# Kernel optimization log

Hardware: AMD Instinct MI355X
Metric: run time of the kernel (lower is better)

## Reference

```python
import jax, jax.numpy as jnp
import numpy as np

EPS = 1e-12  # F.normalize default eps


def build_graph(src, tgt):
    # src,tgt: (b, wh, c). torch does this under no_grad -> stop_gradient.
    logits = jnp.einsum('bnc,bmc->bnm', src, tgt)      # (b, wh, wh)
    g = jax.nn.softmax(logits, axis=-1)                # row softmax
    g = g / jnp.clip(jnp.sum(jnp.abs(g), axis=-2, keepdims=True), EPS)  # L1 norm over dim=-2
    return jax.lax.stop_gradient(g)


def gconv(A, source, message, Wa, ba, Wu, bu):
    # Gconv (PCA-GM style): A @ relu(Linear_a(message)) + relu(Linear_u(source))
    ax = jax.nn.relu(jnp.einsum('bnc,cd->bnd', message, Wa) + ba)
    ux = jax.nn.relu(jnp.einsum('bnc,cd->bnd', source, Wu) + bu)
    return jnp.einsum('bnm,bmd->bnd', A, ax) + ux


def setup_inputs() -> dict:
    key = jax.random.key(0)
    ks = jax.random.split(key, 10)
    b, c, h, w = 4, 256, 64, 64
    scale = 1.0 / np.sqrt(c)
    inp = {
        'skt': jax.random.normal(ks[0], (b, c, h, w), jnp.float32),
        'ref': jax.random.normal(ks[1], (b, c, h, w), jnp.float32),
        'Wa3': jax.random.normal(ks[2], (c, c), jnp.float32) * scale,
        'ba3': jnp.zeros((c,), jnp.float32),
        'Wu3': jax.random.normal(ks[3], (c, c), jnp.float32) * scale,
        'bu3': jnp.zeros((c,), jnp.float32),
        'Wa4': jax.random.normal(ks[4], (c, c), jnp.float32) * scale,
        'ba4': jnp.zeros((c,), jnp.float32),
        'Wu4': jax.random.normal(ks[5], (c, c), jnp.float32) * scale,
        'bu4': jnp.zeros((c,), jnp.float32),
    }
    return inp


def reference(skt, ref, Wa3, ba3, Wu3, bu3, Wa4, ba4, Wu4, bu4):
    b, c, h, w = skt.shape
    skt_f = skt.reshape(b, c, h * w).transpose(0, 2, 1)  # (b, wh, c)
    ref_f = ref.reshape(b, c, h * w).transpose(0, 2, 1)
    sr = build_graph(skt_f, ref_f)                       # (b, wh, wh)
    gen = gconv(sr, skt_f, ref_f, Wa3, ba3, Wu3, bu3) + skt_f
    gg = build_graph(gen, gen)
    ggen = gconv(gg, gen, gen, Wa4, ba4, Wu4, bu4) + gen
    return ggen
```

## Files before the change

### kernel.cpp

```cpp
#include <hip/hip_runtime.h>
#include <cstdint>
#include <cstddef>

#define WH 4096
#define CD 256
typedef long long i64;

typedef __attribute__((ext_vector_type(8))) _Float16 f16x8;
typedef __attribute__((ext_vector_type(4))) float f32x4;

#define AS1 __attribute__((address_space(1)))
#define AS3 __attribute__((address_space(3)))

__device__ __forceinline__ unsigned short f2h(float f) {
    _Float16 h = (_Float16)f;
    return __builtin_bit_cast(unsigned short, h);
}
__device__ __forceinline__ float h2f(unsigned short u) {
    return (float)__builtin_bit_cast(_Float16, u);
}
__device__ __forceinline__ void ld16_lds(const void* g, void* l) {
    __builtin_amdgcn_global_load_lds((AS1 void*)g, (AS3 void*)l, 16, 0, 0);
}

__global__ __launch_bounds__(256) void k_trans(const float* __restrict__ src,
                                               unsigned short* __restrict__ dhi,
                                               unsigned short* __restrict__ dlo,
                                               int RR, int CC, i64 ss, i64 ds) {
    __shared__ float t[32][33];
    const float* s = src + (i64)blockIdx.z * ss;
    const int c0 = blockIdx.x * 32, r0 = blockIdx.y * 32;
    const int tx = threadIdx.x, ty = threadIdx.y;
#pragma unroll
    for (int i = 0; i < 4; ++i)
        t[ty + i * 8][tx] = s[(i64)(r0 + ty + i * 8) * CC + c0 + tx];
    __syncthreads();
#pragma unroll
    for (int i = 0; i < 4; ++i) {
        const i64 idx = (i64)blockIdx.z * ds + (i64)(c0 + ty + i * 8) * RR + r0 + tx;
        const float v = t[tx][ty + i * 8];
        const unsigned short hi = f2h(v);
        dhi[idx] = hi;
        dlo[idx] = f2h(v - h2f(hi));
    }
}

template <int MODE, int SPLIT3>
__global__ __launch_bounds__(256) void k_gemm(
    const unsigned short* __restrict__ A, const unsigned short* __restrict__ A2, int lda, i64 sA,
    const unsigned short* __restrict__ B, const unsigned short* __restrict__ B2, int ldb, i64 sB,
    float* __restrict__ Cf, unsigned short* __restrict__ Chi, unsigned short* __restrict__ Clo,
    int ldc, i64 sC, int K,
    const float* __restrict__ bias,
    const unsigned short* __restrict__ addh, const unsigned short* __restrict__ addl,
    float2* __restrict__ rowP) {
    __shared__ __align__(16) short lA[SPLIT3 ? 8192 : 4096];
    __shared__ __align__(16) short lB[SPLIT3 ? 8192 : 4096];
    __shared__ float2 redp[2][128];
    const int z = blockIdx.z;
    A += (i64)z * sA; B += (i64)z * sB;
    if constexpr (SPLIT3) { A2 += (i64)z * sA; B2 += (i64)z * sB; }

    const int tid = threadIdx.x;
    const int w = tid >> 6, l = tid & 63;
    const int wm = w >> 1, wn = w & 1;
    const int bm = blockIdx.y * 128, bn = blockIdx.x * 128;
    const int l15 = l & 15, lq = l >> 4;

    f32x4 acc[4][4] = {};

    for (int kt = 0; kt < K; kt += 32) {
        __syncthreads();
#pragma unroll
        for (int rr = 0; rr < 2; ++rr) {
            const int r = w + rr * 4;
            const int kb = r >> 1, mh = r & 1;
            const int row = mh * 64 + l;
            const i64 ao = (i64)(bm + row) * lda + kt + kb * 8;
            const i64 bo = (i64)(bn + row) * ldb + kt + kb * 8;
            ld16_lds(A + ao, (char*)lA + r * 1024);
            ld16_lds(B + bo, (char*)lB + r * 1024);
            if constexpr (SPLIT3) {
                ld16_lds(A2 + ao, (char*)lA + 8192 + r * 1024);
                ld16_lds(B2 + bo, (char*)lB + 8192 + r * 1024);
            }
        }
        __syncthreads();
        f16x8 ah[4], bh[4], al[4], bl[4];
#pragma unroll
        for (int i = 0; i < 4; ++i) {
            const int ia = (lq * 128 + wm * 64 + i * 16 + l15) * 8;
            const int ib = (lq * 128 + wn * 64 + i * 16 + l15) * 8;
            ah[i] = *(const f16x8*)(lA + ia);
            bh[i] = *(const f16x8*)(lB + ib);
            if constexpr (SPLIT3) {
                al[i] = *(const f16x8*)(lA + 4096 + ia);
                bl[i] = *(const f16x8*)(lB + 4096 + ib);
            }
        }
#pragma unroll
        for (int i = 0; i < 4; ++i)
#pragma unroll
            for (int j = 0; j < 4; ++j) {
                acc[i][j] = __builtin_amdgcn_mfma_f32_16x16x32_f16(ah[i], bh[j], acc[i][j], 0, 0, 0);
                if constexpr (SPLIT3) {
                    acc[i][j] = __builtin_amdgcn_mfma_f32_16x16x32_f16(ah[i], bl[j], acc[i][j], 0, 0, 0);
                    acc[i][j] = __builtin_amdgcn_mfma_f32_16x16x32_f16(al[i], bh[j], acc[i][j], 0, 0, 0);
                }
            }
    }

#pragma unroll
    for (int i = 0; i < 4; ++i)
#pragma unroll
        for (int j = 0; j < 4; ++j) {
            const int n = bn + wn * 64 + j * 16 + l15;
            const int m0 = bm + wm * 64 + i * 16 + lq * 4;
            float bv = 0.f;
            if constexpr (MODE == 1 || MODE == 2) bv = bias[n];
            if constexpr (MODE == 1) {
                unsigned short hv[4], lv[4];
#pragma unroll
                for (int r = 0; r < 4; ++r) {
                    const float v = fmaxf(acc[i][j][r] + bv, 0.f);
                    hv[r] = f2h(v);
                    lv[r] = f2h(v - h2f(hv[r]));
                }
                const i64 tb = (i64)z * sC + (i64)n * ldc + m0;
                *(ushort4*)(Chi + tb) = make_ushort4(hv[0], hv[1], hv[2], hv[3]);
                *(ushort4*)(Clo + tb) = make_ushort4(lv[0], lv[1], lv[2], lv[3]);
            } else {
#pragma unroll
                for (int r = 0; r < 4; ++r) {
                    float v = acc[i][j][r];
                    const i64 idx = (i64)z * sC + (i64)(m0 + r) * ldc + n;
                    if constexpr (MODE == 0) {
                        Cf[idx] = v;
                    } else {
                        v = fmaxf(v + bv, 0.f);
                        v += h2f(addh[idx]) + h2f(addl[idx]);
                        Cf[idx] = v;
                    }
                }
            }
        }

    if constexpr (MODE == 0) {
        float rm[16], rs[16];
#pragma unroll
        for (int i = 0; i < 4; ++i)
#pragma unroll
            for (int r = 0; r < 4; ++r) {
                float m = fmaxf(fmaxf(acc[i][0][r], acc[i][1][r]), fmaxf(acc[i][2][r], acc[i][3][r]));
                m = fmaxf(m, __shfl_xor(m, 1));
                m = fmaxf(m, __shfl_xor(m, 2));
                m = fmaxf(m, __shfl_xor(m, 4));
                m = fmaxf(m, __shfl_xor(m, 8));
                rm[i * 4 + r] = m;
                float s = __expf(acc[i][0][r] - m) + __expf(acc[i][1][r] - m)
                        + __expf(acc[i][2][r] - m) + __expf(acc[i][3][r] - m);
                s += __shfl_xor(s, 1); s += __shfl_xor(s, 2);
                s += __shfl_xor(s, 4); s += __shfl_xor(s, 8);
                rs[i * 4 + r] = s;
            }
        __syncthreads();
        if (l15 == 0) {
#pragma unroll
            for (int i = 0; i < 4; ++i)
#pragma unroll
                for (int r = 0; r < 4; ++r)
                    redp[wn][wm * 64 + i * 16 + lq * 4 + r] = make_float2(rm[i * 4 + r], rs[i * 4 + r]);
        }
        __syncthreads();
        if (tid < 128) {
            const float2 a = redp[0][tid], b = redp[1][tid];
            const float m = fmaxf(a.x, b.x);
            const float s = a.y * __expf(a.x - m) + b.y * __expf(b.x - m);
            rowP[(i64)blockIdx.x * WH + bm + tid] = make_float2(m, s);
        }
    }
}

__global__ __launch_bounds__(256) void k_colpart(const float* __restrict__ L,
                                                 const float2* __restrict__ rowP,
                                                 float* __restrict__ o,
                                                 float* __restrict__ part) {
    __shared__ float os[64];
    const int t = threadIdx.x;
    const int r0 = blockIdx.y * 64;
    if (t < 64) {
        float M = -3.4e38f, S = 0.f;
        for (int x = 0; x < 32; ++x) {
            const float2 p = rowP[(i64)x * WH + r0 + t];
            const float nm = fmaxf(M, p.x);
            S = S * __expf(M - nm) + p.y * __expf(p.x - nm);
            M = nm;
        }
        const float ov = M + __logf(S);
        os[t] = ov;
        if (blockIdx.x == 0) o[r0 + t] = ov;
    }
    __syncthreads();
    const int j = blockIdx.x * 256 + t;
    float ps = 0.f;
    for (int r = 0; r < 64; ++r)
        ps += __expf(L[(i64)(r0 + r) * WH + j] - os[r]);
    part[(i64)blockIdx.y * WH + j] = ps;
}

__global__ __launch_bounds__(256) void k_colreduce(const float* __restrict__ part,
                                                   float* __restrict__ colS) {
    const int j = blockIdx.x * 256 + threadIdx.x;
    float C = 0.f;
    for (int rb = 0; rb < 64; ++rb) C += part[(i64)rb * WH + j];
    colS[j] = 1.f / fmaxf(C, 1e-12f);
}

template <int FULL>
__global__ __launch_bounds__(256) void k_attn(
    const float* __restrict__ L, const float* __restrict__ o,
    const float* __restrict__ colS,
    const unsigned short* __restrict__ Bh, const unsigned short* __restrict__ Bl,
    unsigned short* __restrict__ Pw) {
    __shared__ __align__(16) float lL[4096];
    __shared__ __align__(16) short lBh[4096];
    __shared__ __align__(16) short lBl[FULL ? 4096 : 64];
    __shared__ float lS[512];
    const int tid = threadIdx.x;
    const int w = tid >> 6, l = tid & 63;
    const int wm = w >> 1, wn = w & 1;
    const int bm = blockIdx.y * 128, bn = blockIdx.x * 128;
    const int l15 = l & 15, lq = l >> 4;
    const i64 koff = (i64)blockIdx.z * 512;

#pragma unroll
    for (int q = 0; q < 2; ++q)
        lS[tid + q * 256] = colS[koff + tid + q * 256];
    float o4[4];
#pragma unroll
    for (int i = 0; i < 4; ++i) o4[i] = o[bm + wm * 64 + i * 16 + l15];

    f32x4 acc[4][4] = {};
    for (int kt = 0; kt < 512; kt += 32) {
        __syncthreads();
#pragma unroll
        for (int rr = 0; rr < 4; ++rr) {
            const int r = w + rr * 4;
            const int kb2 = r >> 1, mh = r & 1;
            ld16_lds(L + (i64)(bm + mh * 64 + l) * WH + koff + kt + kb2 * 4,
                     (char*)lL + r * 1024);
        }
#pragma unroll
        for (int rr = 0; rr < 2; ++rr) {
            const int r = w + rr * 4;
            const int kb = r >> 1, mh = r & 1;
            const i64 bo = (i64)(bn + mh * 64 + l) * WH + koff + kt + kb * 8;
            ld16_lds(Bh + bo, (char*)lBh + r * 1024);
            if constexpr (FULL) ld16_lds(Bl + bo, (char*)lBl + r * 1024);
        }
        __syncthreads();
        float sv[8];
        *(float4*)(sv)     = *(const float4*)(lS + kt + lq * 8);
        *(float4*)(sv + 4) = *(const float4*)(lS + kt + lq * 8 + 4);
        f16x8 bh[4], bl[4];
#pragma unroll
        for (int j = 0; j < 4; ++j) {
            const int ib = (lq * 128 + wn * 64 + j * 16 + l15) * 8;
            bh[j] = *(const f16x8*)(lBh + ib);
            if constexpr (FULL) bl[j] = *(const f16x8*)(lBl + ib);
        }
#pragma unroll
        for (int i = 0; i < 4; ++i) {
            const int mrow = wm * 64 + i * 16 + l15;
            const float* lp = lL + lq * 1024 + mrow * 4;
            float xv[8];
            *(float4*)(xv)     = *(const float4*)(lp);
            *(float4*)(xv + 4) = *(const float4*)(lp + 512);
            const float oi = o4[i];
            f16x8 ah, al;
#pragma unroll
            for (int e = 0; e < 8; ++e) {
                const float a = __expf(xv[e] - oi) * sv[e];
                const _Float16 hh = (_Float16)a;
                ah[e] = hh;
                if constexpr (FULL) al[e] = (_Float16)(a - (float)hh);
            }
#pragma unroll
            for (int j = 0; j < 4; ++j) {
                acc[i][j] = __builtin_amdgcn_mfma_f32_16x16x32_f16(ah, bh[j], acc[i][j], 0, 0, 0);
                if constexpr (FULL) {
                    acc[i][j] = __builtin_amdgcn_mfma_f32_16x16x32_f16(ah, bl[j], acc[i][j], 0, 0, 0);
                    acc[i][j] = __builtin_amdgcn_mfma_f32_16x16x32_f16(al, bh[j], acc[i][j], 0, 0, 0);
                }
            }
        }
    }
    unsigned short* P = Pw + (i64)blockIdx.z * ((i64)WH * CD);
#pragma unroll
    for (int i = 0; i < 4; ++i)
#pragma unroll
        for (int j = 0; j < 4; ++j) {
            const int n = bn + wn * 64 + j * 16 + l15;
            const int m0 = bm + wm * 64 + i * 16 + lq * 4;
#pragma unroll
            for (int r = 0; r < 4; ++r)
                P[(i64)(m0 + r) * CD + n] = f2h(acc[i][j][r]);
        }
}

template <int SPLIT>
__global__ __launch_bounds__(256) void k_red(const unsigned short* __restrict__ Pw,
                                             float* __restrict__ outp,
                                             unsigned short* __restrict__ hi,
                                             unsigned short* __restrict__ lo) {
    const i64 i = ((i64)blockIdx.x * 256 + threadIdx.x) * 4;
    float4 a = *(const float4*)(outp + i);
#pragma unroll
    for (int z = 0; z < 8; ++z) {
        const ushort4 p = *(const ushort4*)(Pw + (i64)z * ((i64)WH * CD) + i);
        a.x += h2f(p.x); a.y += h2f(p.y); a.z += h2f(p.z); a.w += h2f(p.w);
    }
    *(float4*)(outp + i) = a;
    if constexpr (SPLIT) {
        ushort4 h, l2;
        h.x = f2h(a.x); l2.x = f2h(a.x - h2f(h.x));
        h.y = f2h(a.y); l2.y = f2h(a.y - h2f(h.y));
        h.z = f2h(a.z); l2.z = f2h(a.z - h2f(h.z));
        h.w = f2h(a.w); l2.w = f2h(a.w - h2f(h.w));
        *(ushort4*)(hi + i) = h;
        *(ushort4*)(lo + i) = l2;
    }
}

extern "C" void kernel_launch(void* const* d_in, const int* in_sizes, int n_in,
                              void* d_out, int out_size, void* d_ws, size_t ws_size,
                              hipStream_t stream) {
    (void)in_sizes; (void)n_in; (void)out_size; (void)ws_size;
    const float* skt = (const float*)d_in[0];
    const float* ref = (const float*)d_in[1];
    const float* Wa3 = (const float*)d_in[2];
    const float* ba3 = (const float*)d_in[3];
    const float* Wu3 = (const float*)d_in[4];
    const float* bu3 = (const float*)d_in[5];
    const float* Wa4 = (const float*)d_in[6];
    const float* ba4 = (const float*)d_in[7];
    const float* Wu4 = (const float*)d_in[8];
    const float* bu4 = (const float*)d_in[9];
    float* out = (float*)d_out;

    const i64 WHC = (i64)WH * CD;
    const i64 GM  = (i64)WH * WH;
    const i64 CC  = (i64)CD * CD;

    auto al = [](size_t x) { return (x + 255) & ~(size_t)255; };
    char* p = (char*)d_ws; size_t off = 0;
    auto carve = [&](size_t bytes) { void* r = p + off; off += al(bytes); return r; };
    float* Lb             = (float*)carve((size_t)GM * 4);
    unsigned short* skthi = (unsigned short*)carve((size_t)4 * WHC * 2);
    unsigned short* sktlo = (unsigned short*)carve((size_t)4 * WHC * 2);
    unsigned short* refhi = (unsigned short*)carve((size_t)4 * WHC * 2);
    unsigned short* reflo = (unsigned short*)carve((size_t)4 * WHC * 2);
    unsigned short* ghi   = (unsigned short*)carve((size_t)4 * WHC * 2);
    unsigned short* glo   = (unsigned short*)carve((size_t)4 * WHC * 2);
    unsigned short* axthi = (unsigned short*)carve((size_t)4 * WHC * 2);
    unsigned short* axtlo = (unsigned short*)carve((size_t)4 * WHC * 2);
    float* ob             = (float*)carve((size_t)WH * 4);
    float* colS           = (float*)carve((size_t)WH * 4);
    float* partb          = (float*)carve((size_t)64 * WH * 4);
    float2* rowPb         = (float2*)carve((size_t)32 * WH * 8);
    unsigned short* Wthi  = (unsigned short*)carve((size_t)4 * CC * 2);
    unsigned short* Wtlo  = (unsigned short*)carve((size_t)4 * CC * 2);
    unsigned short* Pw    = (unsigned short*)carve((size_t)8 * WHC * 2);

    dim3 thr(256), ttr(32, 8);
    k_trans<<<dim3(WH / 32, CD / 32, 4), ttr, 0, stream>>>(skt, skthi, sktlo, CD, WH, WHC, WHC);
    k_trans<<<dim3(WH / 32, CD / 32, 4), ttr, 0, stream>>>(ref, refhi, reflo, CD, WH, WHC, WHC);
    k_trans<<<dim3(CD / 32, CD / 32, 1), ttr, 0, stream>>>(Wa3, Wthi + 0 * CC, Wtlo + 0 * CC, CD, CD, 0, 0);
    k_trans<<<dim3(CD / 32, CD / 32, 1), ttr, 0, stream>>>(Wu3, Wthi + 1 * CC, Wtlo + 1 * CC, CD, CD, 0, 0);
    k_trans<<<dim3(CD / 32, CD / 32, 1), ttr, 0, stream>>>(Wa4, Wthi + 2 * CC, Wtlo + 2 * CC, CD, CD, 0, 0);
    k_trans<<<dim3(CD / 32, CD / 32, 1), ttr, 0, stream>>>(Wu4, Wthi + 3 * CC, Wtlo + 3 * CC, CD, CD, 0, 0);

    auto stage = [&](const unsigned short* shi, const unsigned short* slo,
                     const unsigned short* mhi, const unsigned short* mlo,
                     int widx, const float* ba, const float* bu, float* outf,
                     unsigned short* ohi, unsigned short* olo, int FULL3) {
        if (FULL3)
            k_gemm<1, 1><<<dim3(CD / 128, WH / 128, 4), thr, 0, stream>>>(
                mhi, mlo, CD, WHC, Wthi + (i64)widx * CC, Wtlo + (i64)widx * CC, CD, 0,
                nullptr, axthi, axtlo, WH, WHC, CD, ba, nullptr, nullptr, nullptr);
        else
            k_gemm<1, 0><<<dim3(CD / 128, WH / 128, 4), thr, 0, stream>>>(
                mhi, nullptr, CD, WHC, Wthi + (i64)widx * CC, nullptr, CD, 0,
                nullptr, axthi, axtlo, WH, WHC, CD, ba, nullptr, nullptr, nullptr);
        if (FULL3)
            k_gemm<2, 1><<<dim3(CD / 128, WH / 128, 4), thr, 0, stream>>>(
                shi, slo, CD, WHC, Wthi + (i64)(widx + 1) * CC, Wtlo + (i64)(widx + 1) * CC, CD, 0,
                outf, nullptr, nullptr, CD, WHC, CD, bu, shi, slo, nullptr);
        else
            k_gemm<2, 0><<<dim3(CD / 128, WH / 128, 4), thr, 0, stream>>>(
                shi, nullptr, CD, WHC, Wthi + (i64)(widx + 1) * CC, nullptr, CD, 0,
                outf, nullptr, nullptr, CD, WHC, CD, bu, shi, slo, nullptr);
        for (int b = 0; b < 4; ++b) {
            k_gemm<0, 1><<<dim3(WH / 128, WH / 128, 1), thr, 0, stream>>>(
                shi + (i64)b * WHC, slo + (i64)b * WHC, CD, 0,
                mhi + (i64)b * WHC, mlo + (i64)b * WHC, CD, 0,
                Lb, nullptr, nullptr, WH, 0, CD, nullptr, nullptr, nullptr, rowPb);
            k_colpart<<<dim3(WH / 256, WH / 64, 1), thr, 0, stream>>>(Lb, rowPb, ob, partb);
            k_colreduce<<<dim3(WH / 256), thr, 0, stream>>>(partb, colS);
            if (FULL3)
                k_attn<1><<<dim3(CD / 128, WH / 128, 8), thr, 0, stream>>>(
                    Lb, ob, colS, axthi + (i64)b * WHC, axtlo + (i64)b * WHC, Pw);
            else
                k_attn<0><<<dim3(CD / 128, WH / 128, 8), thr, 0, stream>>>(
                    Lb, ob, colS, axthi + (i64)b * WHC, nullptr, Pw);
            if (ohi)
                k_red<1><<<dim3((unsigned)(WHC / 1024)), thr, 0, stream>>>(
                    Pw, outf + (i64)b * WHC, ohi + (i64)b * WHC, olo + (i64)b * WHC);
            else
                k_red<0><<<dim3((unsigned)(WHC / 1024)), thr, 0, stream>>>(
                    Pw, outf + (i64)b * WHC, nullptr, nullptr);
        }
    };

    stage(skthi, sktlo, refhi, reflo, 0, ba3, bu3, out, ghi, glo, 1);
    stage(ghi, glo, ghi, glo, 2, ba4, bu4, out, nullptr, nullptr, 0);
}
```

Baseline: 1.081 ms.

## Exploit Gram symmetry in stage-2 logits and widen attention tiles to full feature dim

```diff
diff --git a/kernel.cpp b/kernel.cpp
--- a/kernel.cpp
+++ b/kernel.cpp
@@ -181,6 +181,142 @@
     }
 }
 
+__global__ __launch_bounds__(256) void k_gemm_sym(
+    const unsigned short* __restrict__ A, const unsigned short* __restrict__ A2, int lda,
+    float* __restrict__ Cf, int ldc, int K, float2* __restrict__ rowP) {
+    __shared__ __align__(16) short lA[8192];
+    __shared__ __align__(16) short lB[8192];
+    __shared__ float2 redp[2][128];
+    __shared__ float2 credp[2][128];
+
+    int t = blockIdx.x, by = 0;
+    while (t >= 32 - by) { t -= 32 - by; ++by; }
+    const int bx = by + t;
+    const int bm = by * 128, bn = bx * 128;
+
+    const int tid = threadIdx.x;
+    const int w = tid >> 6, l = tid & 63;
+    const int wm = w >> 1, wn = w & 1;
+    const int l15 = l & 15, lq = l >> 4;
+
+    f32x4 acc[4][4] = {};
+
+    for (int kt = 0; kt < K; kt += 32) {
+        __syncthreads();
+#pragma unroll
+        for (int rr = 0; rr < 2; ++rr) {
+            const int r = w + rr * 4;
+            const int kb = r >> 1, mh = r & 1;
+            const int row = mh * 64 + l;
+            const i64 ao = (i64)(bm + row) * lda + kt + kb * 8;
+            const i64 bo = (i64)(bn + row) * lda + kt + kb * 8;
+            ld16_lds(A + ao, (char*)lA + r * 1024);
+            ld16_lds(A + bo, (char*)lB + r * 1024);
+            ld16_lds(A2 + ao, (char*)lA + 8192 + r * 1024);
+            ld16_lds(A2 + bo, (char*)lB + 8192 + r * 1024);
+        }
+        __syncthreads();
+        f16x8 ah[4], bh[4], al[4], bl[4];
+#pragma unroll
+        for (int i = 0; i < 4; ++i) {
+            const int ia = (lq * 128 + wm * 64 + i * 16 + l15) * 8;
+            const int ib = (lq * 128 + wn * 64 + i * 16 + l15) * 8;
+            ah[i] = *(const f16x8*)(lA + ia);
+            bh[i] = *(const f16x8*)(lB + ib);
+            al[i] = *(const f16x8*)(lA + 4096 + ia);
+            bl[i] = *(const f16x8*)(lB + 4096 + ib);
+        }
+#pragma unroll
+        for (int i = 0; i < 4; ++i)
+#pragma unroll
+            for (int j = 0; j < 4; ++j) {
+                acc[i][j] = __builtin_amdgcn_mfma_f32_16x16x32_f16(ah[i], bh[j], acc[i][j], 0, 0, 0);
+                acc[i][j] = __builtin_amdgcn_mfma_f32_16x16x32_f16(ah[i], bl[j], acc[i][j], 0, 0, 0);
+                acc[i][j] = __builtin_amdgcn_mfma_f32_16x16x32_f16(al[i], bh[j], acc[i][j], 0, 0, 0);
+            }
+    }
+
+#pragma unroll
+    for (int i = 0; i < 4; ++i)
+#pragma unroll
+        for (int j = 0; j < 4; ++j) {
+            const int n = bn + wn * 64 + j * 16 + l15;
+            const int m0 = bm + wm * 64 + i * 16 + lq * 4;
+#pragma unroll
+            for (int r = 0; r < 4; ++r)
+                Cf[(i64)(m0 + r) * ldc + n] = acc[i][j][r];
+            if (bx != by) {
+                float4 tv = make_float4(acc[i][j][0], acc[i][j][1], acc[i][j][2], acc[i][j][3]);
+                *(float4*)(Cf + (i64)n * ldc + m0) = tv;
+            }
+        }
+
+    float rm[16], rs[16];
+#pragma unroll
+    for (int i = 0; i < 4; ++i)
+#pragma unroll
+        for (int r = 0; r < 4; ++r) {
+            float m = fmaxf(fmaxf(acc[i][0][r], acc[i][1][r]), fmaxf(acc[i][2][r], acc[i][3][r]));
+            m = fmaxf(m, __shfl_xor(m, 1));
+            m = fmaxf(m, __shfl_xor(m, 2));
+            m = fmaxf(m, __shfl_xor(m, 4));
+            m = fmaxf(m, __shfl_xor(m, 8));
+            rm[i * 4 + r] = m;
+            float s = __expf(acc[i][0][r] - m) + __expf(acc[i][1][r] - m)
+                    + __expf(acc[i][2][r] - m) + __expf(acc[i][3][r] - m);
+            s += __shfl_xor(s, 1); s += __shfl_xor(s, 2);
+            s += __shfl_xor(s, 4); s += __shfl_xor(s, 8);
+            rs[i * 4 + r] = s;
+        }
+
+    float cm[4], cs[4];
+#pragma unroll
+    for (int j = 0; j < 4; ++j) {
+        float m = -3.4e38f;
+#pragma unroll
+        for (int i = 0; i < 4; ++i)
+#pragma unroll
+            for (int r = 0; r < 4; ++r) m = fmaxf(m, acc[i][j][r]);
+        m = fmaxf(m, __shfl_xor(m, 16));
+        m = fmaxf(m, __shfl_xor(m, 32));
+        float s = 0.f;
+#pragma unroll
+        for (int i = 0; i < 4; ++i)
+#pragma unroll
+            for (int r = 0; r < 4; ++r) s += __expf(acc[i][j][r] - m);
+        s += __shfl_xor(s, 16);
+        s += __shfl_xor(s, 32);
+        cm[j] = m; cs[j] = s;
+    }
+
+    __syncthreads();
+    if (l15 == 0) {
+#pragma unroll
+        for (int i = 0; i < 4; ++i)
+#pragma unroll
+            for (int r = 0; r < 4; ++r)
+                redp[wn][wm * 64 + i * 16 + lq * 4 + r] = make_float2(rm[i * 4 + r], rs[i * 4 + r]);
+    }
+    if (lq == 0) {
+#pragma unroll
+        for (int j = 0; j < 4; ++j)
+            credp[wm][wn * 64 + j * 16 + l15] = make_float2(cm[j], cs[j]);
+    }
+    __syncthreads();
+    if (tid < 128) {
+        float2 a = redp[0][tid], b = redp[1][tid];
+        float m = fmaxf(a.x, b.x);
+        float s = a.y * __expf(a.x - m) + b.y * __expf(b.x - m);
+        rowP[(i64)bx * WH + bm + tid] = make_float2(m, s);
+        if (bx != by) {
+            a = credp[0][tid]; b = credp[1][tid];
+            m = fmaxf(a.x, b.x);
+            s = a.y * __expf(a.x - m) + b.y * __expf(b.x - m);
+            rowP[(i64)by * WH + bn + tid] = make_float2(m, s);
+        }
+    }
+}
+
 __global__ __launch_bounds__(256) void k_colpart(const float* __restrict__ L,
                                                  const float2* __restrict__ rowP,
                                                  float* __restrict__ o,
@@ -222,39 +358,36 @@
     const float* __restrict__ colS,
     const unsigned short* __restrict__ Bh, const unsigned short* __restrict__ Bl,
     unsigned short* __restrict__ Pw) {
-    __shared__ __align__(16) float lL[4096];
-    __shared__ __align__(16) short lBh[4096];
-    __shared__ __align__(16) short lBl[FULL ? 4096 : 64];
+    __shared__ __align__(16) float lL[2048];
+    __shared__ __align__(16) short lBh[8192];
+    __shared__ __align__(16) short lBl[FULL ? 8192 : 8];
     __shared__ float lS[512];
     const int tid = threadIdx.x;
     const int w = tid >> 6, l = tid & 63;
-    const int wm = w >> 1, wn = w & 1;
-    const int bm = blockIdx.y * 128, bn = blockIdx.x * 128;
+    const int bm = blockIdx.x * 64;
     const int l15 = l & 15, lq = l >> 4;
-    const i64 koff = (i64)blockIdx.z * 512;
+    const i64 koff = (i64)blockIdx.y * 512;
 
 #pragma unroll
     for (int q = 0; q < 2; ++q)
         lS[tid + q * 256] = colS[koff + tid + q * 256];
     float o4[4];
 #pragma unroll
-    for (int i = 0; i < 4; ++i) o4[i] = o[bm + wm * 64 + i * 16 + l15];
+    for (int i = 0; i < 4; ++i) o4[i] = o[bm + i * 16 + l15];
 
     f32x4 acc[4][4] = {};
     for (int kt = 0; kt < 512; kt += 32) {
         __syncthreads();
 #pragma unroll
+        for (int rr = 0; rr < 2; ++rr) {
+            const int r = w + rr * 4;
+            ld16_lds(L + (i64)(bm + l) * WH + koff + kt + r * 4, (char*)lL + r * 1024);
+        }
+#pragma unroll
         for (int rr = 0; rr < 4; ++rr) {
             const int r = w + rr * 4;
-            const int kb2 = r >> 1, mh = r & 1;
-            ld16_lds(L + (i64)(bm + mh * 64 + l) * WH + koff + kt + kb2 * 4,
-                     (char*)lL + r * 1024);
-        }
-#pragma unroll
-        for (int rr = 0; rr < 2; ++rr) {
-            const int r = w + rr * 4;
-            const int kb = r >> 1, mh = r & 1;
-            const i64 bo = (i64)(bn + mh * 64 + l) * WH + koff + kt + kb * 8;
+            const int kb = r >> 2, mh = r & 3;
+            const i64 bo = (i64)(mh * 64 + l) * WH + koff + kt + kb * 8;
             ld16_lds(Bh + bo, (char*)lBh + r * 1024);
             if constexpr (FULL) ld16_lds(Bl + bo, (char*)lBl + r * 1024);
         }
@@ -265,17 +398,17 @@
         f16x8 bh[4], bl[4];
 #pragma unroll
         for (int j = 0; j < 4; ++j) {
-            const int ib = (lq * 128 + wn * 64 + j * 16 + l15) * 8;
+            const int ib = (lq * 256 + w * 64 + j * 16 + l15) * 8;
             bh[j] = *(const f16x8*)(lBh + ib);
             if constexpr (FULL) bl[j] = *(const f16x8*)(lBl + ib);
         }
 #pragma unroll
         for (int i = 0; i < 4; ++i) {
-            const int mrow = wm * 64 + i * 16 + l15;
-            const float* lp = lL + lq * 1024 + mrow * 4;
+            const int mrow = i * 16 + l15;
+            const float* lp = lL + lq * 512 + mrow * 4;
             float xv[8];
             *(float4*)(xv)     = *(const float4*)(lp);
-            *(float4*)(xv + 4) = *(const float4*)(lp + 512);
+            *(float4*)(xv + 4) = *(const float4*)(lp + 256);
             const float oi = o4[i];
             f16x8 ah, al;
 #pragma unroll
@@ -295,13 +428,13 @@
             }
         }
     }
-    unsigned short* P = Pw + (i64)blockIdx.z * ((i64)WH * CD);
+    unsigned short* P = Pw + (i64)blockIdx.y * ((i64)WH * CD);
 #pragma unroll
     for (int i = 0; i < 4; ++i)
 #pragma unroll
         for (int j = 0; j < 4; ++j) {
-            const int n = bn + wn * 64 + j * 16 + l15;
-            const int m0 = bm + wm * 64 + i * 16 + lq * 4;
+            const int n = w * 64 + j * 16 + l15;
+            const int m0 = bm + i * 16 + lq * 4;
 #pragma unroll
             for (int r = 0; r < 4; ++r)
                 P[(i64)(m0 + r) * CD + n] = f2h(acc[i][j][r]);
@@ -401,17 +534,21 @@
                 shi, nullptr, CD, WHC, Wthi + (i64)(widx + 1) * CC, nullptr, CD, 0,
                 outf, nullptr, nullptr, CD, WHC, CD, bu, shi, slo, nullptr);
         for (int b = 0; b < 4; ++b) {
-            k_gemm<0, 1><<<dim3(WH / 128, WH / 128, 1), thr, 0, stream>>>(
-                shi + (i64)b * WHC, slo + (i64)b * WHC, CD, 0,
-                mhi + (i64)b * WHC, mlo + (i64)b * WHC, CD, 0,
-                Lb, nullptr, nullptr, WH, 0, CD, nullptr, nullptr, nullptr, rowPb);
+            if (FULL3)
+                k_gemm<0, 1><<<dim3(WH / 128, WH / 128, 1), thr, 0, stream>>>(
+                    shi + (i64)b * WHC, slo + (i64)b * WHC, CD, 0,
+                    mhi + (i64)b * WHC, mlo + (i64)b * WHC, CD, 0,
+                    Lb, nullptr, nullptr, WH, 0, CD, nullptr, nullptr, nullptr, rowPb);
+            else
+                k_gemm_sym<<<dim3(528, 1, 1), thr, 0, stream>>>(
+                    shi + (i64)b * WHC, slo + (i64)b * WHC, CD, Lb, WH, CD, rowPb);
             k_colpart<<<dim3(WH / 256, WH / 64, 1), thr, 0, stream>>>(Lb, rowPb, ob, partb);
             k_colreduce<<<dim3(WH / 256), thr, 0, stream>>>(partb, colS);
             if (FULL3)
-                k_attn<1><<<dim3(CD / 128, WH / 128, 8), thr, 0, stream>>>(
+                k_attn<1><<<dim3(WH / 64, 8, 1), thr, 0, stream>>>(
                     Lb, ob, colS, axthi + (i64)b * WHC, axtlo + (i64)b * WHC, Pw);
             else
-                k_attn<0><<<dim3(CD / 128, WH / 128, 8), thr, 0, stream>>>(
+                k_attn<0><<<dim3(WH / 64, 8, 1), thr, 0, stream>>>(
                     Lb, ob, colS, axthi + (i64)b * WHC, nullptr, Pw);
             if (ohi)
                 k_red<1><<<dim3((unsigned)(WHC / 1024)), thr, 0, stream>>>(
```

New measurement: 1.229 ms. 13.7% more time.

## Fuse split-K reduction into attention via atomics and fold column reduce

Applied to the files above, without the earlier changes.

```diff
diff --git a/kernel.cpp b/kernel.cpp
--- a/kernel.cpp
+++ b/kernel.cpp
@@ -23,12 +23,16 @@
     __builtin_amdgcn_global_load_lds((AS1 void*)g, (AS3 void*)l, 16, 0, 0);
 }
 
-__global__ __launch_bounds__(256) void k_trans(const float* __restrict__ src,
-                                               unsigned short* __restrict__ dhi,
-                                               unsigned short* __restrict__ dlo,
-                                               int RR, int CC, i64 ss, i64 ds) {
+struct TransArgs {
+    const float* src[8];
+    unsigned short* dhi[8];
+    unsigned short* dlo[8];
+};
+__global__ __launch_bounds__(256) void k_transN(TransArgs ta, int RR, int CC) {
     __shared__ float t[32][33];
-    const float* s = src + (i64)blockIdx.z * ss;
+    const float* s = ta.src[blockIdx.z];
+    unsigned short* dhi = ta.dhi[blockIdx.z];
+    unsigned short* dlo = ta.dlo[blockIdx.z];
     const int c0 = blockIdx.x * 32, r0 = blockIdx.y * 32;
     const int tx = threadIdx.x, ty = threadIdx.y;
 #pragma unroll
@@ -37,7 +41,7 @@
     __syncthreads();
 #pragma unroll
     for (int i = 0; i < 4; ++i) {
-        const i64 idx = (i64)blockIdx.z * ds + (i64)(c0 + ty + i * 8) * RR + r0 + tx;
+        const i64 idx = (i64)(c0 + ty + i * 8) * RR + r0 + tx;
         const float v = t[tx][ty + i * 8];
         const unsigned short hi = f2h(v);
         dhi[idx] = hi;
@@ -208,20 +212,12 @@
     part[(i64)blockIdx.y * WH + j] = ps;
 }
 
-__global__ __launch_bounds__(256) void k_colreduce(const float* __restrict__ part,
-                                                   float* __restrict__ colS) {
-    const int j = blockIdx.x * 256 + threadIdx.x;
-    float C = 0.f;
-    for (int rb = 0; rb < 64; ++rb) C += part[(i64)rb * WH + j];
-    colS[j] = 1.f / fmaxf(C, 1e-12f);
-}
-
 template <int FULL>
 __global__ __launch_bounds__(256) void k_attn(
     const float* __restrict__ L, const float* __restrict__ o,
-    const float* __restrict__ colS,
+    const float* __restrict__ part,
     const unsigned short* __restrict__ Bh, const unsigned short* __restrict__ Bl,
-    unsigned short* __restrict__ Pw) {
+    float* __restrict__ Of) {
     __shared__ __align__(16) float lL[4096];
     __shared__ __align__(16) short lBh[4096];
     __shared__ __align__(16) short lBl[FULL ? 4096 : 64];
@@ -233,9 +229,16 @@
     const int l15 = l & 15, lq = l >> 4;
     const i64 koff = (i64)blockIdx.z * 512;
 
-#pragma unroll
-    for (int q = 0; q < 2; ++q)
-        lS[tid + q * 256] = colS[koff + tid + q * 256];
+    {
+        float C0 = 0.f, C1 = 0.f;
+#pragma unroll 4
+        for (int p = 0; p < 64; ++p) {
+            C0 += part[(i64)p * WH + koff + tid];
+            C1 += part[(i64)p * WH + koff + 256 + tid];
+        }
+        lS[tid] = 1.f / fmaxf(C0, 1e-12f);
+        lS[tid + 256] = 1.f / fmaxf(C1, 1e-12f);
+    }
     float o4[4];
 #pragma unroll
     for (int i = 0; i < 4; ++i) o4[i] = o[bm + wm * 64 + i * 16 + l15];
@@ -295,7 +298,6 @@
             }
         }
     }
-    unsigned short* P = Pw + (i64)blockIdx.z * ((i64)WH * CD);
 #pragma unroll
     for (int i = 0; i < 4; ++i)
 #pragma unroll
@@ -304,32 +306,22 @@
             const int m0 = bm + wm * 64 + i * 16 + lq * 4;
 #pragma unroll
             for (int r = 0; r < 4; ++r)
-                P[(i64)(m0 + r) * CD + n] = f2h(acc[i][j][r]);
-        }
-}
-
-template <int SPLIT>
-__global__ __launch_bounds__(256) void k_red(const unsigned short* __restrict__ Pw,
-                                             float* __restrict__ outp,
-                                             unsigned short* __restrict__ hi,
-                                             unsigned short* __restrict__ lo) {
+                unsafeAtomicAdd(Of + (i64)(m0 + r) * CD + n, acc[i][j][r]);
+        }
+}
+
+__global__ __launch_bounds__(256) void k_split(const float* __restrict__ p,
+                                               unsigned short* __restrict__ hi,
+                                               unsigned short* __restrict__ lo) {
     const i64 i = ((i64)blockIdx.x * 256 + threadIdx.x) * 4;
-    float4 a = *(const float4*)(outp + i);
-#pragma unroll
-    for (int z = 0; z < 8; ++z) {
-        const ushort4 p = *(const ushort4*)(Pw + (i64)z * ((i64)WH * CD) + i);
-        a.x += h2f(p.x); a.y += h2f(p.y); a.z += h2f(p.z); a.w += h2f(p.w);
-    }
-    *(float4*)(outp + i) = a;
-    if constexpr (SPLIT) {
-        ushort4 h, l2;
-        h.x = f2h(a.x); l2.x = f2h(a.x - h2f(h.x));
-        h.y = f2h(a.y); l2.y = f2h(a.y - h2f(h.y));
-        h.z = f2h(a.z); l2.z = f2h(a.z - h2f(h.z));
-        h.w = f2h(a.w); l2.w = f2h(a.w - h2f(h.w));
-        *(ushort4*)(hi + i) = h;
-        *(ushort4*)(lo + i) = l2;
-    }
+    const float4 a = *(const float4*)(p + i);
+    ushort4 h, l2;
+    h.x = f2h(a.x); l2.x = f2h(a.x - h2f(h.x));
+    h.y = f2h(a.y); l2.y = f2h(a.y - h2f(h.y));
+    h.z = f2h(a.z); l2.z = f2h(a.z - h2f(h.z));
+    h.w = f2h(a.w); l2.w = f2h(a.w - h2f(h.w));
+    *(ushort4*)(hi + i) = h;
+    *(ushort4*)(lo + i) = l2;
 }
 
 extern "C" void kernel_launch(void* const* d_in, const int* in_sizes, int n_in,
@@ -365,20 +357,29 @@
     unsigned short* axthi = (unsigned short*)carve((size_t)4 * WHC * 2);
     unsigned short* axtlo = (unsigned short*)carve((size_t)4 * WHC * 2);
     float* ob             = (float*)carve((size_t)WH * 4);
-    float* colS           = (float*)carve((size_t)WH * 4);
     float* partb          = (float*)carve((size_t)64 * WH * 4);
     float2* rowPb         = (float2*)carve((size_t)32 * WH * 8);
     unsigned short* Wthi  = (unsigned short*)carve((size_t)4 * CC * 2);
     unsigned short* Wtlo  = (unsigned short*)carve((size_t)4 * CC * 2);
-    unsigned short* Pw    = (unsigned short*)carve((size_t)8 * WHC * 2);
 
     dim3 thr(256), ttr(32, 8);
-    k_trans<<<dim3(WH / 32, CD / 32, 4), ttr, 0, stream>>>(skt, skthi, sktlo, CD, WH, WHC, WHC);
-    k_trans<<<dim3(WH / 32, CD / 32, 4), ttr, 0, stream>>>(ref, refhi, reflo, CD, WH, WHC, WHC);
-    k_trans<<<dim3(CD / 32, CD / 32, 1), ttr, 0, stream>>>(Wa3, Wthi + 0 * CC, Wtlo + 0 * CC, CD, CD, 0, 0);
-    k_trans<<<dim3(CD / 32, CD / 32, 1), ttr, 0, stream>>>(Wu3, Wthi + 1 * CC, Wtlo + 1 * CC, CD, CD, 0, 0);
-    k_trans<<<dim3(CD / 32, CD / 32, 1), ttr, 0, stream>>>(Wa4, Wthi + 2 * CC, Wtlo + 2 * CC, CD, CD, 0, 0);
-    k_trans<<<dim3(CD / 32, CD / 32, 1), ttr, 0, stream>>>(Wu4, Wthi + 3 * CC, Wtlo + 3 * CC, CD, CD, 0, 0);
+    {
+        TransArgs ta{};
+        for (int b = 0; b < 4; ++b) {
+            ta.src[b] = skt + (i64)b * WHC;     ta.src[b + 4] = ref + (i64)b * WHC;
+            ta.dhi[b] = skthi + (i64)b * WHC;   ta.dhi[b + 4] = refhi + (i64)b * WHC;
+            ta.dlo[b] = sktlo + (i64)b * WHC;   ta.dlo[b + 4] = reflo + (i64)b * WHC;
+        }
+        k_transN<<<dim3(WH / 32, CD / 32, 8), ttr, 0, stream>>>(ta, CD, WH);
+        TransArgs tw{};
+        const float* ws[4] = { Wa3, Wu3, Wa4, Wu4 };
+        for (int i = 0; i < 4; ++i) {
+            tw.src[i] = ws[i];
+            tw.dhi[i] = Wthi + (i64)i * CC;
+            tw.dlo[i] = Wtlo + (i64)i * CC;
+        }
+        k_transN<<<dim3(CD / 32, CD / 32, 4), ttr, 0, stream>>>(tw, CD, CD);
+    }
 
     auto stage = [&](const unsigned short* shi, const unsigned short* slo,
                      const unsigned short* mhi, const unsigned short* mlo,
@@ -406,19 +407,17 @@
                 mhi + (i64)b * WHC, mlo + (i64)b * WHC, CD, 0,
                 Lb, nullptr, nullptr, WH, 0, CD, nullptr, nullptr, nullptr, rowPb);
             k_colpart<<<dim3(WH / 256, WH / 64, 1), thr, 0, stream>>>(Lb, rowPb, ob, partb);
-            k_colreduce<<<dim3(WH / 256), thr, 0, stream>>>(partb, colS);
             if (FULL3)
                 k_attn<1><<<dim3(CD / 128, WH / 128, 8), thr, 0, stream>>>(
-                    Lb, ob, colS, axthi + (i64)b * WHC, axtlo + (i64)b * WHC, Pw);
+                    Lb, ob, partb, axthi + (i64)b * WHC, axtlo + (i64)b * WHC,
+                    outf + (i64)b * WHC);
             else
                 k_attn<0><<<dim3(CD / 128, WH / 128, 8), thr, 0, stream>>>(
-                    Lb, ob, colS, axthi + (i64)b * WHC, nullptr, Pw);
+                    Lb, ob, partb, axthi + (i64)b * WHC, nullptr,
+                    outf + (i64)b * WHC);
             if (ohi)
-                k_red<1><<<dim3((unsigned)(WHC / 1024)), thr, 0, stream>>>(
-                    Pw, outf + (i64)b * WHC, ohi + (i64)b * WHC, olo + (i64)b * WHC);
-            else
-                k_red<0><<<dim3((unsigned)(WHC / 1024)), thr, 0, stream>>>(
-                    Pw, outf + (i64)b * WHC, nullptr, nullptr);
+                k_split<<<dim3((unsigned)(WHC / 1024)), thr, 0, stream>>>(
+                    outf + (i64)b * WHC, ohi + (i64)b * WHC, olo + (i64)b * WHC);
         }
     };
 
```

After: 1.210 ms. +11.9%, slower.
